# Optimization experiments

Hardware: AMD Instinct MI355X
Metric: run time of the kernel (lower is better)

The kernel has to match this reference:

```python
import math
import jax, jax.numpy as jnp
import numpy as np

B, H, W, CV = 8, 64, 64, 256
T, CT = 77, 512
NH, TOP_M = 8, 5
CLAMP = 2.0

def _ln(x, g, b, eps=1e-5):
    mu = x.mean(-1, keepdims=True)
    var = ((x - mu) ** 2).mean(-1, keepdims=True)
    return (x - mu) / jnp.sqrt(var + eps) * g + b

def _l2norm(x, eps=1e-6):
    n = jnp.sqrt((x * x).sum(-1, keepdims=True))
    return x / jnp.maximum(n, eps)

def _xavier(key, fan_in, fan_out):
    a = math.sqrt(6.0 / (fan_in + fan_out))
    return jax.random.uniform(key, (fan_in, fan_out), jnp.float32, -a, a)

def setup_inputs() -> dict:
    key = jax.random.key(0)
    ks = jax.random.split(key, 12)
    inp = {
        'visual_features': jax.random.normal(ks[0], (B, H, W, CV), jnp.float32),
        'text_features': jax.random.normal(ks[1], (B, T, CT), jnp.float32),
        'Wq': _xavier(ks[2], CV, CV), 'bq': jnp.zeros((CV,), jnp.float32),
        'Wk': _xavier(ks[3], CT, CV), 'bk': jnp.zeros((CV,), jnp.float32),
        'Wv': _xavier(ks[4], CT, CV), 'bv': jnp.zeros((CV,), jnp.float32),
        'Wo': _xavier(ks[5], CV, CV), 'bo': jnp.zeros((CV,), jnp.float32),
        'g1': jnp.ones((CV,), jnp.float32), 'b1': jnp.zeros((CV,), jnp.float32),
        'g2': jnp.ones((CV,), jnp.float32), 'b2': jnp.zeros((CV,), jnp.float32),
        'W_ffn1': jax.random.normal(ks[6], (CV, 4 * CV), jnp.float32) * 0.02,
        'b_ffn1': jnp.zeros((4 * CV,), jnp.float32),
        'W_ffn2': jax.random.normal(ks[7], (4 * CV, CV), jnp.float32) * 0.02,
        'b_ffn2': jnp.zeros((CV,), jnp.float32),
        'logit_scale': jnp.float32(math.log(1.0 / 0.07)),
        'alpha': jnp.float32(0.1),
    }
    return inp

def _topm_mask(sim, m):
    # keep only top-m entries along last axis (scatter of top-k indices)
    t = sim.shape[-1]
    _, topi = jax.lax.top_k(sim, m)
    keep = jax.vmap(lambda idx: jnp.zeros((t,), bool).at[idx].set(True))(
        topi.reshape(-1, m)).reshape(sim.shape)
    return jnp.where(keep, sim, -jnp.inf)

def _forward(visual_features, text_features, Wq, bq, Wk, bk, Wv, bv, Wo, bo,
             g1, b1, g2, b2, W_ffn1, b_ffn1, W_ffn2, b_ffn2, logit_scale, alpha):
    b, h, w, cv = visual_features.shape
    n = h * w
    dh = cv // NH
    x = _ln(visual_features, g1, b1).reshape(b, n, cv)      # Pre-LN, (B,N,Cv)
    q = (x @ Wq + bq).reshape(b, n, NH, dh)
    k = (text_features @ Wk + bk).reshape(b, T, NH, dh)
    v = (text_features @ Wv + bv).reshape(b, T, NH, dh)
    q = _l2norm(q); k = _l2norm(k)                           # cosine attention
    scale = jnp.exp(jnp.clip(logit_scale, -CLAMP, CLAMP)) / jnp.sqrt(jnp.float32(dh))
    sim = jnp.einsum('bnhd,bthd->bnht', q, k) * scale        # (B,N,H,T)
    pad = jnp.abs(text_features).sum(-1) <= 1e-6             # (B,T) pad tokens
    sim = jnp.where(pad[:, None, None, :], -jnp.inf, sim)
    sim = _topm_mask(sim, TOP_M)
    attn = jax.nn.softmax(sim, axis=-1)
    all_pad = pad.all(axis=1)                                # (B,)
    attn = jnp.where(all_pad[:, None, None, None], 0.0, attn)
    aligned = jnp.einsum('bnht,bthd->bnhd', attn, v).reshape(b, n, cv)
    aligned = aligned @ Wo + bo
    y = x + alpha * aligned
    y = _ln(y, g2, b2)
    hdn = jax.nn.gelu(y @ W_ffn1 + b_ffn1, approximate=False)
    y = y + (hdn @ W_ffn2 + b_ffn2)
    return y.reshape(b, h, w, cv)

def reference(visual_features, text_features, Wq, bq, Wk, bk, Wv, bv, Wo, bo,
              g1, b1, g2, b2, W_ffn1, b_ffn1, W_ffn2, b_ffn2, logit_scale, alpha):
    return _forward(visual_features, text_features, Wq, bq, Wk, bk, Wv, bv, Wo, bo,
                    g1, b1, g2, b2, W_ffn1, b_ffn1, W_ffn2, b_ffn2, logit_scale, alpha)
```

## Files before the change

kernel.cpp:

```cpp
#include <hip/hip_runtime.h>
#include <math.h>

#define NB   8
#define NPIX 4096
#define MROW 32768
#define CV_  256
#define TT   77
#define CT_  512
#define NH_  8
#define DH_  32
#define BT_  616

typedef __bf16 bf16x8 __attribute__((ext_vector_type(8)));
typedef float  f32x4  __attribute__((ext_vector_type(4)));

__device__ __forceinline__ float bf2f(unsigned short u) {
  return __uint_as_float(((unsigned)u) << 16);
}
__device__ __forceinline__ unsigned short f2b(float f) {
  unsigned u = __float_as_uint(f);
  return (unsigned short)((u + 0x7FFFu + ((u >> 16) & 1u)) >> 16);
}
__device__ __forceinline__ unsigned pack2(float lo, float hi) {
  return ((unsigned)f2b(hi) << 16) | (unsigned)f2b(lo);
}
__device__ __forceinline__ void async_copy16(const unsigned short* g,
                                             unsigned short* l) {
  __builtin_amdgcn_global_load_lds(
      (const __attribute__((address_space(1))) void*)g,
      (__attribute__((address_space(3))) void*)l, 16, 0, 0);
}
__device__ __forceinline__ float gelu_t(float v) {
  float p = v * fmaf(0.0713548162726f, v * v, 1.59576912161f);
  float e = __expf(p);
  return v - v / (e + 1.0f);
}

__global__ __launch_bounds__(256) void prep_kernel(
    const float* __restrict__ visual, const float* __restrict__ g1,
    const float* __restrict__ b1, unsigned short* __restrict__ xbuf,
    const float* __restrict__ s0, const float* __restrict__ s1,
    const float* __restrict__ s2, const float* __restrict__ s3,
    const float* __restrict__ s4, const float* __restrict__ s5,
    unsigned short* __restrict__ d0, unsigned short* __restrict__ d1,
    unsigned short* __restrict__ d2, unsigned short* __restrict__ d3,
    unsigned short* __restrict__ d4, unsigned short* __restrict__ d5,
    const float* __restrict__ bk, const float* __restrict__ bv,
    float* __restrict__ bkv, const float* __restrict__ text,
    float* __restrict__ padb) {
  int bx = blockIdx.x;
  int wave = threadIdx.x >> 6, lane = threadIdx.x & 63;
  if (bx < 8192) {
    int row = bx * 4 + wave;
    size_t base = (size_t)row * 256 + lane * 4;
    float4 f = *reinterpret_cast<const float4*>(visual + base);
    float v0 = f.x, v1 = f.y, v2 = f.z, v3 = f.w;
    float s = v0 + v1 + v2 + v3;
    float q = v0 * v0 + v1 * v1 + v2 * v2 + v3 * v3;
#pragma unroll
    for (int off = 1; off < 64; off <<= 1) {
      s += __shfl_xor(s, off);
      q += __shfl_xor(q, off);
    }
    float mean = s * (1.0f / 256.0f);
    float var  = q * (1.0f / 256.0f) - mean * mean;
    float rstd = rsqrtf(var + 1e-5f);
    float4 gv = *reinterpret_cast<const float4*>(g1 + lane * 4);
    float4 bv4 = *reinterpret_cast<const float4*>(b1 + lane * 4);
    ushort4 o;
    o.x = f2b((v0 - mean) * rstd * gv.x + bv4.x);
    o.y = f2b((v1 - mean) * rstd * gv.y + bv4.y);
    o.z = f2b((v2 - mean) * rstd * gv.z + bv4.z);
    o.w = f2b((v3 - mean) * rstd * gv.w + bv4.w);
    *reinterpret_cast<ushort4*>(xbuf + base) = o;
    return;
  }
  if (bx >= 11778) {
    int row = (bx - 11778) * 4 + wave;
    const float* tr = text + (size_t)row * CT_ + lane * 8;
    float4 f0 = *reinterpret_cast<const float4*>(tr);
    float4 f1 = *reinterpret_cast<const float4*>(tr + 4);
    float s = fabsf(f0.x) + fabsf(f0.y) + fabsf(f0.z) + fabsf(f0.w)
            + fabsf(f1.x) + fabsf(f1.y) + fabsf(f1.z) + fabsf(f1.w);
#pragma unroll
    for (int off = 1; off < 64; off <<= 1) s += __shfl_xor(s, off);
    if (lane == 0) padb[row] = (s <= 1e-6f) ? 1.0f : 0.0f;
    return;
  }
  int gi = (bx - 8192) * 256 + threadIdx.x;
  const float* src; unsigned short* dst; int R, C, idx;
  if      (gi < 65536)  { src=s0; dst=d0; R=256;  C=256;  idx=gi; }
  else if (gi < 196608) { src=s1; dst=d1; R=512;  C=256;  idx=gi-65536; }
  else if (gi < 327680) { src=s2; dst=d2; R=512;  C=256;  idx=gi-196608; }
  else if (gi < 393216) { src=s3; dst=d3; R=256;  C=256;  idx=gi-327680; }
  else if (gi < 655360) { src=s4; dst=d4; R=256;  C=1024; idx=gi-393216; }
  else if (gi < 917504) { src=s5; dst=d5; R=1024; C=256;  idx=gi-655360; }
  else if (gi < 918016) {
    int i = gi - 917504;
    bkv[i] = (i < 256) ? bk[i] : bv[i - 256];
    return;
  } else return;
  int r = idx / C, c = idx - r * C;
  dst[(size_t)c * R + r] = f2b(src[idx]);
}

__global__ __launch_bounds__(256) void qkv_kernel(
    const unsigned short* __restrict__ xb, const unsigned short* __restrict__ WqT,
    const float* __restrict__ bq, unsigned short* __restrict__ qout,
    const float* __restrict__ text, const unsigned short* __restrict__ WkvT,
    const float* __restrict__ bkv, float* __restrict__ kout,
    float* __restrict__ vout) {
  __shared__ unsigned short lA[4096];
  __shared__ unsigned short lB[4096];
  int tid = threadIdx.x;
  int lane = tid & 63, wave = tid >> 6;
  int l15 = lane & 15, quad = lane >> 4;
  if (blockIdx.x < 512) {
    int bm = (blockIdx.x >> 1) * 128, bn = (blockIdx.x & 1) * 128;
    int wm = (wave & 1) * 64, wn = (wave >> 1) * 64;
    int crow = lane >> 2, ccol = (lane & 3) * 8;
    f32x4 acc[4][4] = {};
    for (int k0 = 0; k0 < 256; k0 += 32) {
#pragma unroll
      for (int ch = 0; ch < 2; ++ch) {
        int c = wave * 2 + ch;
        async_copy16(xb + (size_t)(bm + c * 16 + crow) * 256 + k0 + ccol,
                     &lA[c * 512]);
        async_copy16(WqT + (size_t)(bn + c * 16 + crow) * 256 + k0 + ccol,
                     &lB[c * 512]);
      }
      __syncthreads();
      bf16x8 af[4], bfr[4];
#pragma unroll
      for (int mi = 0; mi < 4; ++mi)
        af[mi] = *reinterpret_cast<const bf16x8*>(&lA[(wm + mi * 16 + l15) * 32 + quad * 8]);
#pragma unroll
      for (int ni = 0; ni < 4; ++ni)
        bfr[ni] = *reinterpret_cast<const bf16x8*>(&lB[(wn + ni * 16 + l15) * 32 + quad * 8]);
#pragma unroll
      for (int mi = 0; mi < 4; ++mi)
#pragma unroll
        for (int ni = 0; ni < 4; ++ni)
          acc[mi][ni] = __builtin_amdgcn_mfma_f32_16x16x32_bf16(af[mi], bfr[ni],
                                                                acc[mi][ni], 0, 0, 0);
      __syncthreads();
    }
#pragma unroll
    for (int mi = 0; mi < 4; ++mi) {
#pragma unroll
      for (int ni = 0; ni < 4; ++ni) {
        int gcol = bn + wn + ni * 16 + l15;
        float bsf = bq[gcol];
#pragma unroll
        for (int r = 0; r < 4; ++r) {
          int grow = bm + wm + mi * 16 + quad * 4 + r;
          qout[(size_t)grow * 256 + gcol] = f2b(acc[mi][ni][r] + bsf);
        }
      }
    }
  } else {
    int i = blockIdx.x - 512;
    int bm = (i % 10) * 64, bn = (i / 10) * 64;
    int srow = tid >> 2, sc8 = (tid & 3) * 8;
    int wm = (wave & 1) * 32, wn = (wave >> 1) * 32;
    f32x4 acc[2][2] = {};
    int gm = bm + srow, gn = bn + srow;
    const bool aok = (gm < BT_);
    for (int k0 = 0; k0 < CT_; k0 += 32) {
      uint4 apk = make_uint4(0, 0, 0, 0);
      if (aok) {
        const float* Af = text + (size_t)gm * CT_ + k0 + sc8;
        float4 f0 = *reinterpret_cast<const float4*>(Af);
        float4 f1 = *reinterpret_cast<const float4*>(Af + 4);
        apk.x = pack2(f0.x, f0.y); apk.y = pack2(f0.z, f0.w);
        apk.z = pack2(f1.x, f1.y); apk.w = pack2(f1.z, f1.w);
      }
      uint4 bpk = *reinterpret_cast<const uint4*>(WkvT + (size_t)gn * CT_ + k0 + sc8);
      *reinterpret_cast<uint4*>(&lA[srow * 40 + sc8]) = apk;
      *reinterpret_cast<uint4*>(&lB[srow * 40 + sc8]) = bpk;
      __syncthreads();
      bf16x8 a0 = *reinterpret_cast<const bf16x8*>(&lA[(wm + l15) * 40 + quad * 8]);
      bf16x8 a1 = *reinterpret_cast<const bf16x8*>(&lA[(wm + 16 + l15) * 40 + quad * 8]);
      bf16x8 b0 = *reinterpret_cast<const bf16x8*>(&lB[(wn + l15) * 40 + quad * 8]);
      bf16x8 b1 = *reinterpret_cast<const bf16x8*>(&lB[(wn + 16 + l15) * 40 + quad * 8]);
      acc[0][0] = __builtin_amdgcn_mfma_f32_16x16x32_bf16(a0, b0, acc[0][0], 0, 0, 0);
      acc[0][1] = __builtin_amdgcn_mfma_f32_16x16x32_bf16(a0, b1, acc[0][1], 0, 0, 0);
      acc[1][0] = __builtin_amdgcn_mfma_f32_16x16x32_bf16(a1, b0, acc[1][0], 0, 0, 0);
      acc[1][1] = __builtin_amdgcn_mfma_f32_16x16x32_bf16(a1, b1, acc[1][1], 0, 0, 0);
      __syncthreads();
    }
#pragma unroll
    for (int mt = 0; mt < 2; ++mt) {
#pragma unroll
      for (int nt = 0; nt < 2; ++nt) {
        int gcol = bn + wn + nt * 16 + l15;
        float bsf = bkv[gcol];
#pragma unroll
        for (int r = 0; r < 4; ++r) {
          int grow = bm + wm + mt * 16 + quad * 4 + r;
          if (grow >= BT_) continue;
          float v = acc[mt][nt][r] + bsf;
          if (gcol < 256) kout[(size_t)grow * 256 + gcol] = v;
          else            vout[(size_t)grow * 256 + gcol - 256] = v;
        }
      }
    }
  }
}

__global__ __launch_bounds__(256) void gemm_oln(
    const unsigned short* __restrict__ A, const unsigned short* __restrict__ Bt,
    const float* __restrict__ bias, const unsigned short* __restrict__ xres,
    const float* __restrict__ alpha_ptr,
    const float* __restrict__ g2, const float* __restrict__ b2,
    unsigned short* __restrict__ ybf, float* __restrict__ yf32) {
  __shared__ unsigned short sm[32768];
  unsigned short* lA = sm;
  unsigned short* lB = sm + 4096;
  unsigned short* yt = sm;
  const int K = 256;
  int tid = threadIdx.x;
  int bm = blockIdx.x * 128;
  int lane = tid & 63, wave = tid >> 6;
  int wm = (wave & 1) * 64, wn = (wave >> 1) * 128;
  int l15 = lane & 15, quad = lane >> 4;
  int crow = lane >> 2, ccol = (lane & 3) * 8;
  f32x4 acc[4][8] = {};
  for (int k0 = 0; k0 < K; k0 += 32) {
#pragma unroll
    for (int ch = 0; ch < 2; ++ch) {
      int c = wave * 2 + ch;
      async_copy16(A + (size_t)(bm + c * 16 + crow) * K + k0 + ccol,
                   &lA[c * 512]);
    }
#pragma unroll
    for (int ch = wave; ch < 16; ch += 4)
      async_copy16(Bt + (size_t)(ch * 16 + crow) * K + k0 + ccol,
                   &lB[ch * 512]);
    __syncthreads();
    bf16x8 af[4], bfr[8];
#pragma unroll
    for (int mi = 0; mi < 4; ++mi)
      af[mi] = *reinterpret_cast<const bf16x8*>(&lA[(wm + mi * 16 + l15) * 32 + quad * 8]);
#pragma unroll
    for (int ni = 0; ni < 8; ++ni)
      bfr[ni] = *reinterpret_cast<const bf16x8*>(&lB[(wn + ni * 16 + l15) * 32 + quad * 8]);
#pragma unroll
    for (int mi = 0; mi < 4; ++mi)
#pragma unroll
      for (int ni = 0; ni < 8; ++ni)
        acc[mi][ni] = __builtin_amdgcn_mfma_f32_16x16x32_bf16(af[mi], bfr[ni],
                                                              acc[mi][ni], 0, 0, 0);
    __syncthreads();
  }
  float alpha = *alpha_ptr;
#pragma unroll
  for (int mi = 0; mi < 4; ++mi) {
#pragma unroll
    for (int ni = 0; ni < 8; ++ni) {
      int gcol = wn + ni * 16 + l15;
      float bsf = bias[gcol];
#pragma unroll
      for (int r = 0; r < 4; ++r) {
        int lrow = wm + mi * 16 + quad * 4 + r;
        float v = acc[mi][ni][r] + bsf;
        float y0 = bf2f(xres[(size_t)(bm + lrow) * 256 + gcol]) + alpha * v;
        yt[lrow * 256 + gcol] = f2b(y0);
      }
    }
  }
  __syncthreads();
  for (int it = 0; it < 32; ++it) {
    int row = wave * 32 + it;
    ushort4 u = *reinterpret_cast<const ushort4*>(&yt[row * 256 + lane * 4]);
    float v0 = bf2f(u.x), v1 = bf2f(u.y), v2 = bf2f(u.z), v3 = bf2f(u.w);
    float s = v0 + v1 + v2 + v3;
    float q = v0 * v0 + v1 * v1 + v2 * v2 + v3 * v3;
#pragma unroll
    for (int off = 1; off < 64; off <<= 1) {
      s += __shfl_xor(s, off);
      q += __shfl_xor(q, off);
    }
    float mean = s * (1.0f / 256.0f);
    float var  = q * (1.0f / 256.0f) - mean * mean;
    float rstd = rsqrtf(var + 1e-5f);
    float4 gv = *reinterpret_cast<const float4*>(g2 + lane * 4);
    float4 bv = *reinterpret_cast<const float4*>(b2 + lane * 4);
    float o0 = (v0 - mean) * rstd * gv.x + bv.x;
    float o1 = (v1 - mean) * rstd * gv.y + bv.y;
    float o2 = (v2 - mean) * rstd * gv.z + bv.z;
    float o3 = (v3 - mean) * rstd * gv.w + bv.w;
    size_t base = (size_t)(bm + row) * 256 + lane * 4;
    ushort4 ob;
    ob.x = f2b(o0); ob.y = f2b(o1); ob.z = f2b(o2); ob.w = f2b(o3);
    *reinterpret_cast<ushort4*>(ybf + base) = ob;
    *reinterpret_cast<float4*>(yf32 + base) = make_float4(o0, o1, o2, o3);
  }
}

#define SSTR 83
#define VSTR 33
#define NEGBIG -3.0e38f
__device__ __forceinline__ void ins5(float sv, float& tv0, float& tv1,
                                     float& tv2, float& tv3, float& tv4) {
  bool g0 = sv > tv0, g1 = sv > tv1, g2 = sv > tv2, g3 = sv > tv3, g4 = sv > tv4;
  tv4 = g4 ? (g3 ? tv3 : sv) : tv4;
  tv3 = g3 ? (g2 ? tv2 : sv) : tv3;
  tv2 = g2 ? (g1 ? tv1 : sv) : tv2;
  tv1 = g1 ? (g0 ? tv0 : sv) : tv1;
  tv0 = g0 ? sv : tv0;
}
__global__ __launch_bounds__(256) void attn_kernel(
    unsigned short* qa, const float* __restrict__ k,
    const float* __restrict__ v, const float* __restrict__ padb,
    const float* __restrict__ ls_ptr) {
  __shared__ unsigned short qb[64 * 40];
  __shared__ unsigned short kb[80 * 40];
  __shared__ float S[64 * SSTR];
  __shared__ float vs[TT * VSTR];
  __shared__ float rn[64];
  __shared__ float scs[80];
  __shared__ int allpad_s;
  int tid = threadIdx.x;
  int h = blockIdx.y, b = blockIdx.z;
  size_t qbase = ((size_t)b * NPIX + blockIdx.x * 64) * CV_ + h * DH_;
  size_t kvbase = (size_t)b * TT * CV_ + h * DH_;
  float ls = *ls_ptr;
  ls = fminf(fmaxf(ls, -2.0f), 2.0f);
  float scale = expf(ls) * 0.17677669529663687f;
  if (tid == 0) allpad_s = 1;
  __syncthreads();
  int qrow = tid >> 2, qq = tid & 3;
  uint4 qv4 = *reinterpret_cast<const uint4*>(qa + qbase + (size_t)qrow * CV_ + qq * 8);
  *reinterpret_cast<uint4*>(&qb[qrow * 40 + qq * 8]) = qv4;
  {
    float ssq = 0.f;
    unsigned w[4] = {qv4.x, qv4.y, qv4.z, qv4.w};
#pragma unroll
    for (int i = 0; i < 4; ++i) {
      float a = bf2f((unsigned short)(w[i] & 0xFFFF));
      float bb = bf2f((unsigned short)(w[i] >> 16));
      ssq += a * a + bb * bb;
    }
    ssq += __shfl_xor(ssq, 1);
    ssq += __shfl_xor(ssq, 2);
    if (qq == 0) rn[qrow] = scale / fmaxf(sqrtf(ssq), 1e-6f);
  }
  if (tid < 154) {
    int kr = tid >> 1, kh = tid & 1;
    const float* kp = k + kvbase + (size_t)kr * CV_ + kh * 16;
    float4 f0 = *reinterpret_cast<const float4*>(kp);
    float4 f1 = *reinterpret_cast<const float4*>(kp + 4);
    float4 f2 = *reinterpret_cast<const float4*>(kp + 8);
    float4 f3 = *reinterpret_cast<const float4*>(kp + 12);
    float ks2 = f0.x*f0.x + f0.y*f0.y + f0.z*f0.z + f0.w*f0.w
              + f1.x*f1.x + f1.y*f1.y + f1.z*f1.z + f1.w*f1.w
              + f2.x*f2.x + f2.y*f2.y + f2.z*f2.z + f2.w*f2.w
              + f3.x*f3.x + f3.y*f3.y + f3.z*f3.z + f3.w*f3.w;
    uint4 p0, p1;
    p0.x = pack2(f0.x, f0.y); p0.y = pack2(f0.z, f0.w);
    p0.z = pack2(f1.x, f1.y); p0.w = pack2(f1.z, f1.w);
    p1.x = pack2(f2.x, f2.y); p1.y = pack2(f2.z, f2.w);
    p1.z = pack2(f3.x, f3.y); p1.w = pack2(f3.z, f3.w);
    *reinterpret_cast<uint4*>(&kb[kr * 40 + kh * 16]) = p0;
    *reinterpret_cast<uint4*>(&kb[kr * 40 + kh * 16 + 8]) = p1;
    ks2 += __shfl_xor(ks2, 1);
    if (kh == 0) {
      float p = padb[b * TT + kr];
      float sc = (p == 0.0f) ? 1.0f / fmaxf(sqrtf(ks2), 1e-6f) : 0.0f;
      scs[kr] = sc;
      if (sc > 0.0f) allpad_s = 0;
    }
  } else if (tid < 157) {
    scs[77 + (tid - 154)] = 0.0f;
  } else if (tid >= 160 && tid < 172) {
    int i = tid - 160;
    *reinterpret_cast<uint4*>(&kb[(77 + (i >> 2)) * 40 + (i & 3) * 8]) =
        make_uint4(0, 0, 0, 0);
  }
  for (int j = tid; j < TT * 8; j += 256) {
    int t = j >> 3, d4 = j & 7;
    float4 f = *reinterpret_cast<const float4*>(
        v + kvbase + (size_t)t * CV_ + d4 * 4);
    float* vp = &vs[t * VSTR + d4 * 4];
    vp[0] = f.x; vp[1] = f.y; vp[2] = f.z; vp[3] = f.w;
  }
  __syncthreads();
  {
    int lane = tid & 63, wave = tid >> 6;
    int wm = wave * 16;
    int l15 = lane & 15, quad = lane >> 4;
    f32x4 acc[5] = {};
    bf16x8 af = *reinterpret_cast<const bf16x8*>(&qb[(wm + l15) * 40 + quad * 8]);
    bf16x8 bfr[5];
#pragma unroll
    for (int ni = 0; ni < 5; ++ni)
      bfr[ni] = *reinterpret_cast<const bf16x8*>(&kb[(ni * 16 + l15) * 40 + quad * 8]);
#pragma unroll
    for (int ni = 0; ni < 5; ++ni)
      acc[ni] = __builtin_amdgcn_mfma_f32_16x16x32_bf16(af, bfr[ni], acc[ni], 0, 0, 0);
#pragma unroll
    for (int ni = 0; ni < 5; ++ni) {
      int col = ni * 16 + l15;
      float sc = scs[col];
#pragma unroll
      for (int r = 0; r < 4; ++r) {
        int row = wm + quad * 4 + r;
        float val = (sc > 0.0f) ? acc[ni][r] * rn[row] * sc : NEGBIG;
        unsigned pb = (__float_as_uint(val) & 0xFFFFFF80u) | (unsigned)col;
        S[row * SSTR + col] = __uint_as_float(pb);
      }
    }
  }
  __syncthreads();
  int allpad = allpad_s;
  int row = qrow;
  const float* Srow = &S[row * SSTR];
  int t0 = qq * 20, t1 = (qq == 3) ? TT : t0 + 20;
  float tv0 = -INFINITY, tv1 = -INFINITY, tv2 = -INFINITY,
        tv3 = -INFINITY, tv4 = -INFINITY;
  for (int t = t0; t < t1; ++t)
    ins5(Srow[t], tv0, tv1, tv2, tv3, tv4);
#pragma unroll
  for (int m = 1; m <= 2; m <<= 1) {
    float n0 = __shfl_xor(tv0, m), n1 = __shfl_xor(tv1, m),
          n2 = __shfl_xor(tv2, m), n3 = __shfl_xor(tv3, m),
          n4 = __shfl_xor(tv4, m);
    ins5(n0, tv0, tv1, tv2, tv3, tv4);
    ins5(n1, tv0, tv1, tv2, tv3, tv4);
    ins5(n2, tv0, tv1, tv2, tv3, tv4);
    ins5(n3, tv0, tv1, tv2, tv3, tv4);
    ins5(n4, tv0, tv1, tv2, tv3, tv4);
  }
  float o[8];
#pragma unroll
  for (int d = 0; d < 8; ++d) o[d] = 0.f;
  if (!allpad) {
    float e0 = 1.0f;
    float e1 = expf(tv1 - tv0);
    float e2 = expf(tv2 - tv0);
    float e3 = expf(tv3 - tv0);
    float e4 = expf(tv4 - tv0);
    float inv = 1.0f / (e0 + e1 + e2 + e3 + e4);
    int i0 = __float_as_uint(tv0) & 0x7F, i1 = __float_as_uint(tv1) & 0x7F,
        i2 = __float_as_uint(tv2) & 0x7F, i3 = __float_as_uint(tv3) & 0x7F,
        i4 = __float_as_uint(tv4) & 0x7F;
    const float* v0p = &vs[i0 * VSTR + qq * 8];
    const float* v1p = &vs[i1 * VSTR + qq * 8];
    const float* v2p = &vs[i2 * VSTR + qq * 8];
    const float* v3p = &vs[i3 * VSTR + qq * 8];
    const float* v4p = &vs[i4 * VSTR + qq * 8];
#pragma unroll
    for (int d = 0; d < 8; ++d)
      o[d] = (e0 * v0p[d] + e1 * v1p[d] + e2 * v2p[d] + e3 * v3p[d] + e4 * v4p[d]) * inv;
  }
  unsigned short* qp = qa + qbase + (size_t)row * CV_ + qq * 8;
  uint4 ou;
  ou.x = ((unsigned)f2b(o[1]) << 16) | f2b(o[0]);
  ou.y = ((unsigned)f2b(o[3]) << 16) | f2b(o[2]);
  ou.z = ((unsigned)f2b(o[5]) << 16) | f2b(o[4]);
  ou.w = ((unsigned)f2b(o[7]) << 16) | f2b(o[6]);
  *reinterpret_cast<uint4*>(qp) = ou;
}

#define XSTR 264
#define HSTR 136
__global__ __launch_bounds__(512) void ffn_fused(
    const unsigned short* __restrict__ ybf, const unsigned short* __restrict__ W1T,
    const float* __restrict__ b1f, const unsigned short* __restrict__ W2T,
    const float* __restrict__ b2f, float* __restrict__ yio) {
  __shared__ unsigned short xs[128 * XSTR];
  __shared__ unsigned short Hs[128 * HSTR];
  __shared__ unsigned short Wb[16384];
  int tid = threadIdx.x, lane = tid & 63, wave = tid >> 6;
  int l15 = lane & 15, quad = lane >> 4;
  int crow = lane >> 2, ccol = (lane & 3) * 8;
  int bm = blockIdx.x * 128;
  {
    int row = tid >> 2, kh = (tid & 3) * 64;
    const unsigned short* src = ybf + (size_t)(bm + row) * 256 + kh;
    unsigned short* dst = &xs[row * XSTR + kh];
#pragma unroll
    for (int i = 0; i < 8; ++i)
      *reinterpret_cast<uint4*>(dst + i * 8) =
          *reinterpret_cast<const uint4*>(src + i * 8);
  }
  int wm2 = (wave & 1) * 64, wn2 = (wave >> 1) * 64;
  int wh1 = (wave & 1) * 64, wr1 = (wave >> 1) * 32;
  f32x4 acc[4][4] = {};
  for (int c = 0; c < 8; ++c) {
    f32x4 acc1[4][2] = {};
    for (int slab = 0; slab < 2; ++slab) {
      int k0 = slab * 128;
      __syncthreads();
#pragma unroll
      for (int s = 0; s < 4; ++s)
        async_copy16(W1T + (size_t)(c * 128 + wave * 16 + crow) * 256
                         + k0 + s * 32 + ccol,
                     &Wb[s * 4096 + wave * 512]);
      __syncthreads();
#pragma unroll
      for (int s = 0; s < 4; ++s) {
        bf16x8 af[4], bfr[2];
#pragma unroll
        for (int mi = 0; mi < 4; ++mi)
          af[mi] = *reinterpret_cast<const bf16x8*>(
              &Wb[s * 4096 + (wh1 + mi * 16 + l15) * 32 + quad * 8]);
#pragma unroll
        for (int ni = 0; ni < 2; ++ni)
          bfr[ni] = *reinterpret_cast<const bf16x8*>(
              &xs[(wr1 + ni * 16 + l15) * XSTR + k0 + s * 32 + quad * 8]);
#pragma unroll
        for (int mi = 0; mi < 4; ++mi)
#pragma unroll
          for (int ni = 0; ni < 2; ++ni)
            acc1[mi][ni] = __builtin_amdgcn_mfma_f32_16x16x32_bf16(
                af[mi], bfr[ni], acc1[mi][ni], 0, 0, 0);
      }
    }
#pragma unroll
    for (int mi = 0; mi < 4; ++mi) {
      int hb = wh1 + mi * 16 + quad * 4;
      float b0 = b1f[c * 128 + hb],     b1v = b1f[c * 128 + hb + 1];
      float b2v = b1f[c * 128 + hb + 2], b3 = b1f[c * 128 + hb + 3];
#pragma unroll
      for (int ni = 0; ni < 2; ++ni) {
        int row = wr1 + ni * 16 + l15;
        ushort4 hw;
        hw.x = f2b(gelu_t(acc1[mi][ni][0] + b0));
        hw.y = f2b(gelu_t(acc1[mi][ni][1] + b1v));
        hw.z = f2b(gelu_t(acc1[mi][ni][2] + b2v));
        hw.w = f2b(gelu_t(acc1[mi][ni][3] + b3));
        *reinterpret_cast<ushort4*>(&Hs[row * HSTR + hb]) = hw;
      }
    }
#pragma unroll
    for (int j = 0; j < 2; ++j) {
      __syncthreads();
#pragma unroll
      for (int u = 0; u < 2; ++u)
#pragma unroll
        for (int i = 0; i < 2; ++i) {
          int ch = wave * 2 + i;
          async_copy16(W2T + (size_t)(ch * 16 + crow) * 1024
                           + c * 128 + j * 64 + u * 32 + ccol,
                       &Wb[u * 8192 + ch * 512]);
        }
      __syncthreads();
#pragma unroll
      for (int u = 0; u < 2; ++u) {
        int kk = j * 64 + u * 32;
        bf16x8 af[4], bfr[4];
#pragma unroll
        for (int mi = 0; mi < 4; ++mi)
          af[mi] = *reinterpret_cast<const bf16x8*>(
              &Hs[(wm2 + mi * 16 + l15) * HSTR + kk + quad * 8]);
#pragma unroll
        for (int ni = 0; ni < 4; ++ni)
          bfr[ni] = *reinterpret_cast<const bf16x8*>(
              &Wb[u * 8192 + (wn2 + ni * 16 + l15) * 32 + quad * 8]);
#pragma unroll
        for (int mi = 0; mi < 4; ++mi)
#pragma unroll
          for (int ni = 0; ni < 4; ++ni)
            acc[mi][ni] = __builtin_amdgcn_mfma_f32_16x16x32_bf16(
                af[mi], bfr[ni], acc[mi][ni], 0, 0, 0);
      }
    }
  }
#pragma unroll
  for (int mi = 0; mi < 4; ++mi)
#pragma unroll
    for (int ni = 0; ni < 4; ++ni) {
      int col = wn2 + ni * 16 + l15;
      float bs = b2f[col];
#pragma unroll
      for (int r = 0; r < 4; ++r) {
        int g = bm + wm2 + mi * 16 + quad * 4 + r;
        size_t oi = (size_t)g * 256 + col;
        yio[oi] = yio[oi] + acc[mi][ni][r] + bs;
      }
    }
}

extern "C" void kernel_launch(void* const* d_in, const int* in_sizes, int n_in,
                              void* d_out, int out_size, void* d_ws, size_t ws_size,
                              hipStream_t stream) {
  const float* visual = (const float*)d_in[0];
  const float* text   = (const float*)d_in[1];
  const float* Wq  = (const float*)d_in[2];
  const float* bq  = (const float*)d_in[3];
  const float* Wk  = (const float*)d_in[4];
  const float* bk  = (const float*)d_in[5];
  const float* Wv  = (const float*)d_in[6];
  const float* bv  = (const float*)d_in[7];
  const float* Wo  = (const float*)d_in[8];
  const float* bo  = (const float*)d_in[9];
  const float* g1  = (const float*)d_in[10];
  const float* b1  = (const float*)d_in[11];
  const float* g2  = (const float*)d_in[12];
  const float* b2  = (const float*)d_in[13];
  const float* W1  = (const float*)d_in[14];
  const float* bf1 = (const float*)d_in[15];
  const float* W2  = (const float*)d_in[16];
  const float* bff2 = (const float*)d_in[17];
  const float* lsc = (const float*)d_in[18];
  const float* alp = (const float*)d_in[19];

  char* ws = (char*)d_ws;
  size_t off = 0;
  auto alloc = [&](size_t bytes) -> char* {
    char* p = ws + off;
    off += (bytes + 255) & ~(size_t)255;
    return p;
  };
  unsigned short* WqT = (unsigned short*)alloc((size_t)65536 * 2);
  unsigned short* WkT = (unsigned short*)alloc((size_t)131072 * 2);
  unsigned short* WvT = (unsigned short*)alloc((size_t)131072 * 2);
  unsigned short* WoT = (unsigned short*)alloc((size_t)65536 * 2);
  unsigned short* W1T = (unsigned short*)alloc((size_t)262144 * 2);
  unsigned short* W2T = (unsigned short*)alloc((size_t)262144 * 2);
  float*          bkv  = (float*)alloc(512 * 4);
  float*          kbuf = (float*)alloc((size_t)BT_ * CV_ * 4);
  float*          vbuf = (float*)alloc((size_t)BT_ * CV_ * 4);
  float*          padb = (float*)alloc((size_t)BT_ * 4);
  char* U = ws + off;
  unsigned short* xbuf = (unsigned short*)U;
  unsigned short* qbuf = (unsigned short*)(U + 16777216);
  float*          ybuf = (float*)d_out;

  prep_kernel<<<11932, 256, 0, stream>>>(visual, g1, b1, xbuf,
                                         Wq, Wk, Wv, Wo, W1, W2,
                                         WqT, WkT, WvT, WoT, W1T, W2T,
                                         bk, bv, bkv, text, padb);
  qkv_kernel<<<592, 256, 0, stream>>>(xbuf, WqT, bq, qbuf,
                                      text, WkT, bkv, kbuf, vbuf);
  attn_kernel<<<dim3(64, NH_, NB), 256, 0, stream>>>(qbuf, kbuf, vbuf, padb, lsc);
  gemm_oln<<<256, 256, 0, stream>>>(qbuf, WoT, bo, xbuf, alp, g2, b2,
                                    xbuf, ybuf);
  ffn_fused<<<256, 512, 0, stream>>>(xbuf, W1T, bf1, W2T, bff2, ybuf);
}
```

Measured before the change: 300.5 us.

## Double-buffer FFN weight loads with swizzled LDS and halve gemm_oln tile rows

The fused FFN kernel now streams W1/W2 weight slabs through a two-stage double-buffered LDS pipeline. The next slab's async copy is issued while the current one is computed, using manual waitcnt/barriers, an XOR-swizzled LDS layout to avoid bank conflicts, and raised wave priority around the MFMA blocks. Separately, gemm_oln uses 64-row tiles instead of 128, doubling the grid to 512 blocks for better CU occupancy and lower LDS use. The pipelining depends on correct vmcnt accounting and the swizzle matching on both the copy and read sides, which adds correctness risk.

```diff
diff --git a/kernel.cpp b/kernel.cpp
--- a/kernel.cpp
+++ b/kernel.cpp
@@ -214,39 +214,35 @@
     const float* __restrict__ alpha_ptr,
     const float* __restrict__ g2, const float* __restrict__ b2,
     unsigned short* __restrict__ ybf, float* __restrict__ yf32) {
-  __shared__ unsigned short sm[32768];
+  __shared__ unsigned short sm[16384];
   unsigned short* lA = sm;
-  unsigned short* lB = sm + 4096;
+  unsigned short* lB = sm + 2048;
   unsigned short* yt = sm;
   const int K = 256;
   int tid = threadIdx.x;
-  int bm = blockIdx.x * 128;
+  int bm = blockIdx.x * 64;
   int lane = tid & 63, wave = tid >> 6;
-  int wm = (wave & 1) * 64, wn = (wave >> 1) * 128;
+  int wm = (wave & 1) * 32, wn = (wave >> 1) * 128;
   int l15 = lane & 15, quad = lane >> 4;
   int crow = lane >> 2, ccol = (lane & 3) * 8;
-  f32x4 acc[4][8] = {};
+  f32x4 acc[2][8] = {};
   for (int k0 = 0; k0 < K; k0 += 32) {
-#pragma unroll
-    for (int ch = 0; ch < 2; ++ch) {
-      int c = wave * 2 + ch;
-      async_copy16(A + (size_t)(bm + c * 16 + crow) * K + k0 + ccol,
-                   &lA[c * 512]);
-    }
+    async_copy16(A + (size_t)(bm + wave * 16 + crow) * K + k0 + ccol,
+                 &lA[wave * 512]);
 #pragma unroll
     for (int ch = wave; ch < 16; ch += 4)
       async_copy16(Bt + (size_t)(ch * 16 + crow) * K + k0 + ccol,
                    &lB[ch * 512]);
     __syncthreads();
-    bf16x8 af[4], bfr[8];
-#pragma unroll
-    for (int mi = 0; mi < 4; ++mi)
+    bf16x8 af[2], bfr[8];
+#pragma unroll
+    for (int mi = 0; mi < 2; ++mi)
       af[mi] = *reinterpret_cast<const bf16x8*>(&lA[(wm + mi * 16 + l15) * 32 + quad * 8]);
 #pragma unroll
     for (int ni = 0; ni < 8; ++ni)
       bfr[ni] = *reinterpret_cast<const bf16x8*>(&lB[(wn + ni * 16 + l15) * 32 + quad * 8]);
 #pragma unroll
-    for (int mi = 0; mi < 4; ++mi)
+    for (int mi = 0; mi < 2; ++mi)
 #pragma unroll
       for (int ni = 0; ni < 8; ++ni)
         acc[mi][ni] = __builtin_amdgcn_mfma_f32_16x16x32_bf16(af[mi], bfr[ni],
@@ -255,7 +251,7 @@
   }
   float alpha = *alpha_ptr;
 #pragma unroll
-  for (int mi = 0; mi < 4; ++mi) {
+  for (int mi = 0; mi < 2; ++mi) {
 #pragma unroll
     for (int ni = 0; ni < 8; ++ni) {
       int gcol = wn + ni * 16 + l15;
@@ -270,8 +266,8 @@
     }
   }
   __syncthreads();
-  for (int it = 0; it < 32; ++it) {
-    int row = wave * 32 + it;
+  for (int it = 0; it < 16; ++it) {
+    int row = wave * 16 + it;
     ushort4 u = *reinterpret_cast<const ushort4*>(&yt[row * 256 + lane * 4]);
     float v0 = bf2f(u.x), v1 = bf2f(u.y), v2 = bf2f(u.z), v3 = bf2f(u.w);
     float s = v0 + v1 + v2 + v3;
@@ -474,7 +470,9 @@
   __shared__ unsigned short Wb[16384];
   int tid = threadIdx.x, lane = tid & 63, wave = tid >> 6;
   int l15 = lane & 15, quad = lane >> 4;
-  int crow = lane >> 2, ccol = (lane & 3) * 8;
+  int crow = lane >> 2;
+  int ccs = (((lane & 3) ^ ((lane >> 3) & 3)) * 8);
+  int rsw = ((quad ^ ((l15 >> 1) & 3)) * 8);
   int bm = blockIdx.x * 128;
   {
     int row = tid >> 2, kh = (tid & 3) * 64;
@@ -487,69 +485,78 @@
   }
   int wm2 = (wave & 1) * 64, wn2 = (wave >> 1) * 64;
   int wh1 = (wave & 1) * 64, wr1 = (wave >> 1) * 32;
+  auto stage = [&](int st) {
+    st &= 63;
+    int c = st >> 3, p = st & 7;
+    unsigned short* buf = &Wb[(st & 1) * 8192];
+    if (p < 4) {
+#pragma unroll
+      for (int sl = 0; sl < 2; ++sl)
+        async_copy16(W1T + (size_t)(c * 128 + wave * 16 + crow) * 256
+                         + p * 64 + sl * 32 + ccs,
+                     &buf[sl * 4096 + wave * 512]);
+    } else {
+      int q = p - 4;
+#pragma unroll
+      for (int i = 0; i < 2; ++i)
+        async_copy16(W2T + (size_t)((wave * 2 + i) * 16 + crow) * 1024
+                         + c * 128 + q * 32 + ccs,
+                     &buf[(wave * 2 + i) * 512]);
+    }
+  };
   f32x4 acc[4][4] = {};
+  stage(0); stage(1);
   for (int c = 0; c < 8; ++c) {
     f32x4 acc1[4][2] = {};
-    for (int slab = 0; slab < 2; ++slab) {
-      int k0 = slab * 128;
-      __syncthreads();
-#pragma unroll
-      for (int s = 0; s < 4; ++s)
-        async_copy16(W1T + (size_t)(c * 128 + wave * 16 + crow) * 256
-                         + k0 + s * 32 + ccol,
-                     &Wb[s * 4096 + wave * 512]);
-      __syncthreads();
-#pragma unroll
-      for (int s = 0; s < 4; ++s) {
-        bf16x8 af[4], bfr[2];
-#pragma unroll
-        for (int mi = 0; mi < 4; ++mi)
-          af[mi] = *reinterpret_cast<const bf16x8*>(
-              &Wb[s * 4096 + (wh1 + mi * 16 + l15) * 32 + quad * 8]);
-#pragma unroll
-        for (int ni = 0; ni < 2; ++ni)
-          bfr[ni] = *reinterpret_cast<const bf16x8*>(
-              &xs[(wr1 + ni * 16 + l15) * XSTR + k0 + s * 32 + quad * 8]);
-#pragma unroll
-        for (int mi = 0; mi < 4; ++mi)
+#pragma unroll
+    for (int p = 0; p < 8; ++p) {
+      int st = c * 8 + p;
+      asm volatile("s_waitcnt vmcnt(2) lgkmcnt(0)" ::: "memory");
+      __builtin_amdgcn_s_barrier();
+      __builtin_amdgcn_sched_barrier(0);
+      const unsigned short* buf = &Wb[(p & 1) * 8192];
+      if (p < 4) {
+#pragma unroll
+        for (int sl = 0; sl < 2; ++sl) {
+          int k = p * 64 + sl * 32;
+          bf16x8 af[4], bfr[2];
+#pragma unroll
+          for (int mi = 0; mi < 4; ++mi)
+            af[mi] = *reinterpret_cast<const bf16x8*>(
+                &buf[sl * 4096 + (wh1 + mi * 16 + l15) * 32 + rsw]);
 #pragma unroll
           for (int ni = 0; ni < 2; ++ni)
-            acc1[mi][ni] = __builtin_amdgcn_mfma_f32_16x16x32_bf16(
-                af[mi], bfr[ni], acc1[mi][ni], 0, 0, 0);
-      }
-    }
-#pragma unroll
-    for (int mi = 0; mi < 4; ++mi) {
-      int hb = wh1 + mi * 16 + quad * 4;
-      float b0 = b1f[c * 128 + hb],     b1v = b1f[c * 128 + hb + 1];
-      float b2v = b1f[c * 128 + hb + 2], b3 = b1f[c * 128 + hb + 3];
-#pragma unroll
-      for (int ni = 0; ni < 2; ++ni) {
-        int row = wr1 + ni * 16 + l15;
-        ushort4 hw;
-        hw.x = f2b(gelu_t(acc1[mi][ni][0] + b0));
-        hw.y = f2b(gelu_t(acc1[mi][ni][1] + b1v));
-        hw.z = f2b(gelu_t(acc1[mi][ni][2] + b2v));
-        hw.w = f2b(gelu_t(acc1[mi][ni][3] + b3));
-        *reinterpret_cast<ushort4*>(&Hs[row * HSTR + hb]) = hw;
-      }
-    }
-#pragma unroll
-    for (int j = 0; j < 2; ++j) {
-      __syncthreads();
-#pragma unroll
-      for (int u = 0; u < 2; ++u)
-#pragma unroll
-        for (int i = 0; i < 2; ++i) {
-          int ch = wave * 2 + i;
-          async_copy16(W2T + (size_t)(ch * 16 + crow) * 1024
-                           + c * 128 + j * 64 + u * 32 + ccol,
-                       &Wb[u * 8192 + ch * 512]);
+            bfr[ni] = *reinterpret_cast<const bf16x8*>(
+                &xs[(wr1 + ni * 16 + l15) * XSTR + k + quad * 8]);
+          __builtin_amdgcn_s_setprio(1);
+#pragma unroll
+          for (int mi = 0; mi < 4; ++mi)
+#pragma unroll
+            for (int ni = 0; ni < 2; ++ni)
+              acc1[mi][ni] = __builtin_amdgcn_mfma_f32_16x16x32_bf16(
+                  af[mi], bfr[ni], acc1[mi][ni], 0, 0, 0);
+          __builtin_amdgcn_s_setprio(0);
         }
-      __syncthreads();
-#pragma unroll
-      for (int u = 0; u < 2; ++u) {
-        int kk = j * 64 + u * 32;
+        if (p == 3) {
+#pragma unroll
+          for (int mi = 0; mi < 4; ++mi) {
+            int hb = wh1 + mi * 16 + quad * 4;
+            float b0 = b1f[c * 128 + hb],      b1v = b1f[c * 128 + hb + 1];
+            float b2v = b1f[c * 128 + hb + 2], b3 = b1f[c * 128 + hb + 3];
+#pragma unroll
+            for (int ni = 0; ni < 2; ++ni) {
+              int row = wr1 + ni * 16 + l15;
+              ushort4 hw;
+              hw.x = f2b(gelu_t(acc1[mi][ni][0] + b0));
+              hw.y = f2b(gelu_t(acc1[mi][ni][1] + b1v));
+              hw.z = f2b(gelu_t(acc1[mi][ni][2] + b2v));
+              hw.w = f2b(gelu_t(acc1[mi][ni][3] + b3));
+              *reinterpret_cast<ushort4*>(&Hs[row * HSTR + hb]) = hw;
+            }
+          }
+        }
+      } else {
+        int q = p - 4, kk = q * 32;
         bf16x8 af[4], bfr[4];
 #pragma unroll
         for (int mi = 0; mi < 4; ++mi)
@@ -558,16 +565,23 @@
 #pragma unroll
         for (int ni = 0; ni < 4; ++ni)
           bfr[ni] = *reinterpret_cast<const bf16x8*>(
-              &Wb[u * 8192 + (wn2 + ni * 16 + l15) * 32 + quad * 8]);
+              &buf[(wn2 + ni * 16 + l15) * 32 + rsw]);
+        __builtin_amdgcn_s_setprio(1);
 #pragma unroll
         for (int mi = 0; mi < 4; ++mi)
 #pragma unroll
           for (int ni = 0; ni < 4; ++ni)
             acc[mi][ni] = __builtin_amdgcn_mfma_f32_16x16x32_bf16(
                 af[mi], bfr[ni], acc[mi][ni], 0, 0, 0);
-      }
-    }
-  }
+        __builtin_amdgcn_s_setprio(0);
+      }
+      __builtin_amdgcn_sched_barrier(0);
+      __builtin_amdgcn_s_barrier();
+      __builtin_amdgcn_sched_barrier(0);
+      stage(st + 2);
+    }
+  }
+  asm volatile("s_waitcnt vmcnt(0)" ::: "memory");
 #pragma unroll
   for (int mi = 0; mi < 4; ++mi)
 #pragma unroll
@@ -636,7 +650,7 @@
   qkv_kernel<<<592, 256, 0, stream>>>(xbuf, WqT, bq, qbuf,
                                       text, WkT, bkv, kbuf, vbuf);
   attn_kernel<<<dim3(64, NH_, NB), 256, 0, stream>>>(qbuf, kbuf, vbuf, padb, lsc);
-  gemm_oln<<<256, 256, 0, stream>>>(qbuf, WoT, bo, xbuf, alp, g2, b2,
+  gemm_oln<<<512, 256, 0, stream>>>(qbuf, WoT, bo, xbuf, alp, g2, b2,
                                     xbuf, ybuf);
   ffn_fused<<<256, 512, 0, stream>>>(xbuf, W1T, bf1, W2T, bff2, ybuf);
 }
```

Result: faster. 287.2 us (-4.4%).
